# Kernel optimization log

Measured on AMD Instinct MI355X. Metric: run time of the kernel, lower is better.

Reference implementation:

```python
import jax, jax.numpy as jnp
import numpy as np
import math

H, HD = 16, 64
EPS = 1e-6


def setup_inputs() -> dict:
    key = jax.random.key(0)
    ks = jax.random.split(key, 6)
    B, T, D = 4, 2048, 1024
    s = 0.02
    return {
        "x": jax.random.normal(ks[0], (B, T, D), jnp.float32),
        "wq": jax.random.normal(ks[1], (D, D), jnp.float32) * s,
        "wk": jax.random.normal(ks[2], (D, D), jnp.float32) * s,
        "wv": jax.random.normal(ks[3], (D, D), jnp.float32) * s,
        "wo": jax.random.normal(ks[4], (D, D), jnp.float32) * s,
        "norm_g": jnp.ones((D,), jnp.float32),
    }


def reference(x, wq, wk, wv, wo, norm_g):
    B, T, D = x.shape
    scale = math.sqrt(HD)
    # nn.Linear(D, D, bias=False): y = x @ W.T
    q = (x @ wq.T).reshape(B, T, H, HD).transpose(0, 2, 1, 3)  # [B,H,T,HD]
    k = (x @ wk.T).reshape(B, T, H, HD).transpose(0, 2, 1, 3)
    v = (x @ wv.T).reshape(B, T, H, HD).transpose(0, 2, 1, 3)
    scores = jnp.einsum("bhqd,bhkd->bhqk", q, k) / scale  # [B,H,T,T]
    causal = jnp.tril(jnp.ones((T, T), bool))  # True where allowed
    scores = jnp.where(causal, scores, -jnp.inf)
    attn = jax.nn.softmax(scores, axis=-1)  # dropout p=0 -> identity
    out = jnp.einsum("bhqk,bhkd->bhqd", attn, v)  # [B,H,T,HD]
    out = out.transpose(0, 2, 1, 3).reshape(B, T, D)
    y = x + out @ wo.T  # residual
    # RMSNorm
    rms = jnp.sqrt(jnp.mean(y * y, axis=-1, keepdims=True) + EPS)
    return (y / rms) * norm_g
```

## Files before the change

### kernel.cpp

```cpp
#include <hip/hip_runtime.h>
#include <hip/hip_bf16.h>

constexpr int NB  = 4;
constexpr int NT  = 2048;
constexpr int ND  = 1024;
constexpr int NH  = 16;
constexpr int NHD = 64;
constexpr int NM  = NB * NT;

typedef unsigned short u16;
typedef __attribute__((ext_vector_type(8))) short  short8;
typedef __attribute__((ext_vector_type(4))) float  f32x4;

__device__ __forceinline__ u16 f2bf(float f) {
  unsigned u = __builtin_bit_cast(unsigned, f);
  u += 0x7FFFu + ((u >> 16) & 1u);
  return (u16)(u >> 16);
}

__device__ __forceinline__ unsigned pk2bf(float lo, float hi_) {
  float2 t; t.x = lo; t.y = hi_;
  __hip_bfloat162 h2 = __float22bfloat162_rn(t);
  unsigned u;
  __builtin_memcpy(&u, &h2, 4);
  return u;
}

__device__ __forceinline__ void gll16(const u16* src, u16* dst) {
  __builtin_amdgcn_global_load_lds(
      (const __attribute__((address_space(1))) void*)src,
      (__attribute__((address_space(3))) void*)dst, 16, 0, 0);
}

__global__ __launch_bounds__(256) void cast_kernel(const float* __restrict__ in,
                                                   u16* __restrict__ out, int n4) {
  int i = blockIdx.x * 256 + threadIdx.x;
  if (i >= n4) return;
  float4 v = ((const float4*)in)[i];
  ushort4 o;
  o.x = f2bf(v.x); o.y = f2bf(v.y); o.z = f2bf(v.z); o.w = f2bf(v.w);
  ((ushort4*)out)[i] = o;
}

__global__ __launch_bounds__(256) void gemm_qkv(
    const u16* __restrict__ xb,
    const u16* __restrict__ wqb, const u16* __restrict__ wkb, const u16* __restrict__ wvb,
    u16* __restrict__ Qb, u16* __restrict__ Kb, u16* __restrict__ VTb) {
  const int z = blockIdx.z;
  const u16* wsel = (z == 0) ? wqb : (z == 1) ? wkb : wvb;
  u16* osel      = (z == 0) ? Qb  : (z == 1) ? Kb  : VTb;
  const float scl = (z == 0) ? 0.125f * 1.44269504f : 1.0f;

  const int row0 = blockIdx.x * 128;
  const int col0 = blockIdx.y * 128;
  const int tid  = threadIdx.x;
  const int lane = tid & 63, wid = tid >> 6;
  const int wm = wid >> 1, wn = wid & 1;
  const int li = lane & 15, hi = lane >> 4;

  __shared__ __align__(16) u16 lA[128 * 32];
  __shared__ __align__(16) u16 lB[128 * 32];

  f32x4 acc[4][4] = {};
  const int rl = lane >> 2;
  const int c8 = lane & 3;

  for (int k0 = 0; k0 < ND; k0 += 32) {
#pragma unroll
    for (int h = 0; h < 2; ++h) {
      int r = wid * 32 + h * 16 + rl;
      gll16(&xb  [(size_t)(row0 + r) * ND + k0 + c8 * 8], &lA[(wid * 32 + h * 16) * 32]);
      gll16(&wsel[(size_t)(col0 + r) * ND + k0 + c8 * 8], &lB[(wid * 32 + h * 16) * 32]);
    }
    __syncthreads();
    short8 a[4], b[4];
#pragma unroll
    for (int m = 0; m < 4; ++m)
      a[m] = *(const short8*)&lA[(wm * 64 + m * 16 + li) * 32 + hi * 8];
#pragma unroll
    for (int n = 0; n < 4; ++n)
      b[n] = *(const short8*)&lB[(wn * 64 + n * 16 + li) * 32 + hi * 8];
    if (z == 2) {
#pragma unroll
      for (int m = 0; m < 4; ++m)
#pragma unroll
        for (int n = 0; n < 4; ++n)
          acc[m][n] = __builtin_amdgcn_mfma_f32_16x16x32_bf16(a[m], b[n], acc[m][n], 0, 0, 0);
    } else {
#pragma unroll
      for (int m = 0; m < 4; ++m)
#pragma unroll
        for (int n = 0; n < 4; ++n)
          acc[m][n] = __builtin_amdgcn_mfma_f32_16x16x32_bf16(b[n], a[m], acc[m][n], 0, 0, 0);
    }
    __syncthreads();
  }

#pragma unroll
  for (int m = 0; m < 4; ++m)
#pragma unroll
    for (int n = 0; n < 4; ++n) {
      if (z == 2) {
        int token0 = row0 + wm * 64 + m * 16 + hi * 4;
        int col    = col0 + wn * 64 + n * 16 + li;
        int b_ = token0 >> 11, t0 = token0 & (NT - 1);
        int h_ = col >> 6,     d_ = col & (NHD - 1);
        uint2 w;
        w.x = pk2bf(acc[m][n][0], acc[m][n][1]);
        w.y = pk2bf(acc[m][n][2], acc[m][n][3]);
        *(uint2*)&osel[(((size_t)(b_ * NH + h_)) * NHD + d_) * NT + t0] = w;
      } else {
        int token = row0 + wm * 64 + m * 16 + li;
        int feat0 = col0 + wn * 64 + n * 16 + hi * 4;
        int b_ = token >> 11, t_ = token & (NT - 1);
        int h_ = feat0 >> 6,  d0 = feat0 & (NHD - 1);
        uint2 w;
        w.x = pk2bf(acc[m][n][0] * scl, acc[m][n][1] * scl);
        w.y = pk2bf(acc[m][n][2] * scl, acc[m][n][3] * scl);
        *(uint2*)&osel[(((size_t)(b_ * NH + h_)) * NT + t_) * NHD + d0] = w;
      }
    }
}

__global__ __launch_bounds__(256) void gemm_wo(
    const u16* __restrict__ ao, const u16* __restrict__ wob,
    const float* __restrict__ x, float* __restrict__ y) {
  const int row0 = blockIdx.x * 128;
  const int col0 = blockIdx.y * 128;
  const int tid  = threadIdx.x;
  const int lane = tid & 63, wid = tid >> 6;
  const int wm = wid >> 1, wn = wid & 1;
  const int li = lane & 15, hi = lane >> 4;

  __shared__ __align__(16) u16 lA[128 * 32];
  __shared__ __align__(16) u16 lB[128 * 32];

  f32x4 acc[4][4] = {};
  const int rl = lane >> 2;
  const int c8 = lane & 3;

  for (int k0 = 0; k0 < ND; k0 += 32) {
#pragma unroll
    for (int h = 0; h < 2; ++h) {
      int r = wid * 32 + h * 16 + rl;
      gll16(&ao [(size_t)(row0 + r) * ND + k0 + c8 * 8], &lA[(wid * 32 + h * 16) * 32]);
      gll16(&wob[(size_t)(col0 + r) * ND + k0 + c8 * 8], &lB[(wid * 32 + h * 16) * 32]);
    }
    __syncthreads();
    short8 a[4], b[4];
#pragma unroll
    for (int m = 0; m < 4; ++m)
      a[m] = *(const short8*)&lA[(wm * 64 + m * 16 + li) * 32 + hi * 8];
#pragma unroll
    for (int n = 0; n < 4; ++n)
      b[n] = *(const short8*)&lB[(wn * 64 + n * 16 + li) * 32 + hi * 8];
#pragma unroll
    for (int m = 0; m < 4; ++m)
#pragma unroll
      for (int n = 0; n < 4; ++n)
        acc[m][n] = __builtin_amdgcn_mfma_f32_16x16x32_bf16(b[n], a[m], acc[m][n], 0, 0, 0);
    __syncthreads();
  }

#pragma unroll
  for (int m = 0; m < 4; ++m)
#pragma unroll
    for (int n = 0; n < 4; ++n) {
      int token = row0 + wm * 64 + m * 16 + li;
      int feat0 = col0 + wn * 64 + n * 16 + hi * 4;
      size_t idx = (size_t)token * ND + feat0;
      float4 xv = *(const float4*)&x[idx];
      float4 o;
      o.x = acc[m][n][0] + xv.x; o.y = acc[m][n][1] + xv.y;
      o.z = acc[m][n][2] + xv.z; o.w = acc[m][n][3] + xv.w;
      *(float4*)&y[idx] = o;
    }
}

__global__ __launch_bounds__(256) void attn_kernel(
    const u16* __restrict__ Q, const u16* __restrict__ K, const u16* __restrict__ VT,
    u16* __restrict__ AO) {
  const int nb  = gridDim.x * gridDim.y;
  const int b0  = blockIdx.y * gridDim.x + blockIdx.x;
  const int L   = (b0 & 7) * (nb >> 3) + (b0 >> 3);
  const int qb  = 31 - (L & 31);
  const int bh  = L >> 5;

  const int tid = threadIdx.x;
  const int lane = tid & 63, wid = tid >> 6;
  const int li = lane & 15, hi = lane >> 4;
  const int r0 = qb * 64 + wid * 16;
  const int qrow = r0 + li;
  const size_t bK = (size_t)bh * NT * NHD;
  const size_t bV = (size_t)bh * NHD * NT;

  __shared__ __align__(16) u16 lK [2][64 * 64];
  __shared__ __align__(16) u16 lVT[2][64 * 64];
  __shared__ __align__(16) u16 lP [4][16 * 64];

  const int ch0 = tid, ch1 = tid + 256;
  const int d0 = (ch0 >> 3) * 64 + (((ch0 & 7) ^ ((ch0 >> 3) & 7)) << 3);
  const int d1 = (ch1 >> 3) * 64 + (((ch1 & 7) ^ ((ch1 >> 3) & 7)) << 3);
  const int vOff0 = (ch0 >> 3) * NT + (ch0 & 7) * 8;
  const int vOff1 = (ch1 >> 3) * NT + (ch1 & 7) * 8;

  uint4 gK0, gK1, gV0, gV1;
  auto issue = [&](int kt) {
    const u16* kp = K + bK + (size_t)kt * 4096;
    const u16* vp = VT + bV + kt * 64;
    gK0 = *(const uint4*)&kp[ch0 * 8];
    gK1 = *(const uint4*)&kp[ch1 * 8];
    gV0 = *(const uint4*)&vp[vOff0];
    gV1 = *(const uint4*)&vp[vOff1];
  };
  auto commit = [&](int buf) {
    *(uint4*)&lK [buf][d0] = gK0;
    *(uint4*)&lK [buf][d1] = gK1;
    *(uint4*)&lVT[buf][d0] = gV0;
    *(uint4*)&lVT[buf][d1] = gV1;
  };

  short8 qf[2];
#pragma unroll
  for (int c = 0; c < 2; ++c)
    qf[c] = *(const short8*)&Q[bK + (size_t)qrow * NHD + c * 32 + hi * 8];

  short8 vone;
#pragma unroll
  for (int e = 0; e < 8; ++e) vone[e] = (short)0x3F80;

  f32x4 o[4] = {};
  f32x4 o4 = {};
  float mr = -INFINITY;

  issue(0);
  commit(0);
  __syncthreads();
  int buf = 0;

  const int pswz = (li & 7) << 1;

  for (int kt = 0; kt <= qb; ++kt) {
    if (kt < qb) issue(kt + 1);

    f32x4 s[4] = {};
    __builtin_amdgcn_s_setprio(1);
#pragma unroll
    for (int g = 0; g < 4; ++g)
#pragma unroll
      for (int c = 0; c < 2; ++c) {
        short8 kf = *(const short8*)&lK[buf][(g * 16 + li) * 64 + ((c * 4 + hi) ^ (li & 7)) * 8];
        s[g] = __builtin_amdgcn_mfma_f32_16x16x32_bf16(kf, qf[c], s[g], 0, 0, 0);
      }
    __builtin_amdgcn_s_setprio(0);

    if (kt == qb) {
#pragma unroll
      for (int g = 0; g < 4; ++g)
#pragma unroll
        for (int rg = 0; rg < 4; ++rg) {
          int kcol = kt * 64 + g * 16 + hi * 4 + rg;
          if (kcol > qrow) s[g][rg] = -INFINITY;
        }
    }

    float mg0 = fmaxf(fmaxf(s[0][0], s[0][1]), fmaxf(s[0][2], s[0][3]));
    float mg1 = fmaxf(fmaxf(s[1][0], s[1][1]), fmaxf(s[1][2], s[1][3]));
    float mg2 = fmaxf(fmaxf(s[2][0], s[2][1]), fmaxf(s[2][2], s[2][3]));
    float mg3 = fmaxf(fmaxf(s[3][0], s[3][1]), fmaxf(s[3][2], s[3][3]));
    float pmax = fmaxf(fmaxf(mg0, mg1), fmaxf(mg2, mg3));
    pmax = fmaxf(pmax, __shfl_xor(pmax, 16));
    pmax = fmaxf(pmax, __shfl_xor(pmax, 32));

    if (__any(pmax > mr + 8.f)) {
      float mnew = fmaxf(mr, pmax);
      float sc = __builtin_amdgcn_exp2f(mr - mnew);
#pragma unroll
      for (int gd = 0; gd < 4; ++gd)
#pragma unroll
        for (int rg = 0; rg < 4; ++rg) o[gd][rg] *= sc;
#pragma unroll
      for (int rg = 0; rg < 4; ++rg) o4[rg] *= sc;
      mr = mnew;
    }

#pragma unroll
    for (int g = 0; g < 4; ++g) {
      float p0 = __builtin_amdgcn_exp2f(s[g][0] - mr);
      float p1 = __builtin_amdgcn_exp2f(s[g][1] - mr);
      float p2 = __builtin_amdgcn_exp2f(s[g][2] - mr);
      float p3 = __builtin_amdgcn_exp2f(s[g][3] - mr);
      uint2 w;
      w.x = pk2bf(p0, p1);
      w.y = pk2bf(p2, p3);
      int k8s = (g * 4 + hi) ^ pswz;
      *(uint2*)&lP[wid][li * 64 + k8s * 4] = w;
    }

    short8 pa[2];
#pragma unroll
    for (int c = 0; c < 2; ++c)
      pa[c] = *(const short8*)&lP[wid][li * 64 + ((c * 8 + hi * 2) ^ pswz) * 4];

    __builtin_amdgcn_s_setprio(1);
#pragma unroll
    for (int gd = 0; gd < 4; ++gd)
#pragma unroll
      for (int c = 0; c < 2; ++c) {
        short8 vf = *(const short8*)&lVT[buf][(gd * 16 + li) * 64 + ((c * 4 + hi) ^ (li & 7)) * 8];
        o[gd] = __builtin_amdgcn_mfma_f32_16x16x32_bf16(vf, pa[c], o[gd], 0, 0, 0);
      }
#pragma unroll
    for (int c = 0; c < 2; ++c)
      o4 = __builtin_amdgcn_mfma_f32_16x16x32_bf16(vone, pa[c], o4, 0, 0, 0);
    __builtin_amdgcn_s_setprio(0);

    if (kt < qb) commit(buf ^ 1);
    __syncthreads();
    buf ^= 1;
  }

  const int b_ = bh >> 4, h_ = bh & 15;
  const float inv = 1.0f / o4[0];
  const size_t rowbase = ((size_t)(b_ * NT + qrow)) * ND + h_ * 64;
#pragma unroll
  for (int gd = 0; gd < 4; ++gd) {
    uint2 w;
    w.x = pk2bf(o[gd][0] * inv, o[gd][1] * inv);
    w.y = pk2bf(o[gd][2] * inv, o[gd][3] * inv);
    *(uint2*)&AO[rowbase + gd * 16 + hi * 4] = w;
  }
}

__global__ __launch_bounds__(256) void rmsnorm_kernel(float* __restrict__ y,
                                                      const float* __restrict__ g) {
  const int row = blockIdx.x;
  const int tid = threadIdx.x;
  const int lane = tid & 63, wid = tid >> 6;
  float4 v = ((const float4*)(y + (size_t)row * ND))[tid];
  float ss = v.x * v.x + v.y * v.y + v.z * v.z + v.w * v.w;
#pragma unroll
  for (int off = 32; off; off >>= 1) ss += __shfl_down(ss, off);
  __shared__ float red[4];
  if (lane == 0) red[wid] = ss;
  __syncthreads();
  float tot = red[0] + red[1] + red[2] + red[3];
  float inv = rsqrtf(tot * (1.0f / (float)ND) + 1e-6f);
  float4 gg = ((const float4*)g)[tid];
  float4 o;
  o.x = v.x * inv * gg.x; o.y = v.y * inv * gg.y;
  o.z = v.z * inv * gg.z; o.w = v.w * inv * gg.w;
  ((float4*)(y + (size_t)row * ND))[tid] = o;
}

extern "C" void kernel_launch(void* const* d_in, const int* in_sizes, int n_in,
                              void* d_out, int out_size, void* d_ws, size_t ws_size,
                              hipStream_t stream) {
  const float* x  = (const float*)d_in[0];
  const float* wq = (const float*)d_in[1];
  const float* wk = (const float*)d_in[2];
  const float* wv = (const float*)d_in[3];
  const float* wo = (const float*)d_in[4];
  const float* ng = (const float*)d_in[5];
  float* out = (float*)d_out;

  char* ws = (char*)d_ws;
  u16* xb  = (u16*)(ws);
  u16* wqb = (u16*)(ws + (16u << 20));
  u16* wkb = (u16*)(ws + (18u << 20));
  u16* wvb = (u16*)(ws + (20u << 20));
  u16* wob = (u16*)(ws + (22u << 20));
  u16* Qb  = (u16*)(ws + (24u << 20));
  u16* Kb  = (u16*)(ws + (40u << 20));
  u16* VTb = (u16*)(ws + (56u << 20));
  u16* AO  = (u16*)(ws + (72u << 20));

  cast_kernel<<<NM * ND / 4 / 256, 256, 0, stream>>>(x,  xb,  NM * ND / 4);
  cast_kernel<<<ND * ND / 4 / 256, 256, 0, stream>>>(wq, wqb, ND * ND / 4);
  cast_kernel<<<ND * ND / 4 / 256, 256, 0, stream>>>(wk, wkb, ND * ND / 4);
  cast_kernel<<<ND * ND / 4 / 256, 256, 0, stream>>>(wv, wvb, ND * ND / 4);
  cast_kernel<<<ND * ND / 4 / 256, 256, 0, stream>>>(wo, wob, ND * ND / 4);

  gemm_qkv<<<dim3(NM / 128, ND / 128, 3), 256, 0, stream>>>(xb, wqb, wkb, wvb, Qb, Kb, VTb);
  attn_kernel<<<dim3(NT / 64, NB * NH), 256, 0, stream>>>(Qb, Kb, VTb, AO);
  gemm_wo<<<dim3(NM / 128, ND / 128), 256, 0, stream>>>(AO, wob, x, out);
  rmsnorm_kernel<<<NM, 256, 0, stream>>>(out, ng);
}
```

Baseline: 227.0 us.

## Double GEMM K-tile with XOR-swizzled LDS, XCD-aware block remap, fuse weight casts

```diff
diff --git a/kernel.cpp b/kernel.cpp
--- a/kernel.cpp
+++ b/kernel.cpp
@@ -42,56 +42,84 @@
   ((ushort4*)out)[i] = o;
 }
 
+__global__ __launch_bounds__(256) void cast4_kernel(
+    const float* __restrict__ w0, const float* __restrict__ w1,
+    const float* __restrict__ w2, const float* __restrict__ w3,
+    u16* __restrict__ o0, u16* __restrict__ o1,
+    u16* __restrict__ o2, u16* __restrict__ o3) {
+  const int z = blockIdx.x >> 10;
+  const float* in = (z == 0) ? w0 : (z == 1) ? w1 : (z == 2) ? w2 : w3;
+  u16* out       = (z == 0) ? o0 : (z == 1) ? o1 : (z == 2) ? o2 : o3;
+  int i = (blockIdx.x & 1023) * 256 + threadIdx.x;
+  float4 v = ((const float4*)in)[i];
+  ushort4 o;
+  o.x = f2bf(v.x); o.y = f2bf(v.y); o.z = f2bf(v.z); o.w = f2bf(v.w);
+  ((ushort4*)out)[i] = o;
+}
+
 __global__ __launch_bounds__(256) void gemm_qkv(
     const u16* __restrict__ xb,
     const u16* __restrict__ wqb, const u16* __restrict__ wkb, const u16* __restrict__ wvb,
     u16* __restrict__ Qb, u16* __restrict__ Kb, u16* __restrict__ VTb) {
-  const int z = blockIdx.z;
+  const int nwg  = 64 * 8 * 3;
+  const int flat = (blockIdx.z * 8 + blockIdx.y) * 64 + blockIdx.x;
+  const int L    = (flat & 7) * (nwg >> 3) + (flat >> 3);
+  const int z    = L / 512;
+  const int rem  = L & 511;
+  const int col0 = (rem >> 6) << 7;
+  const int row0 = (rem & 63) << 7;
+
   const u16* wsel = (z == 0) ? wqb : (z == 1) ? wkb : wvb;
   u16* osel      = (z == 0) ? Qb  : (z == 1) ? Kb  : VTb;
   const float scl = (z == 0) ? 0.125f * 1.44269504f : 1.0f;
 
-  const int row0 = blockIdx.x * 128;
-  const int col0 = blockIdx.y * 128;
   const int tid  = threadIdx.x;
   const int lane = tid & 63, wid = tid >> 6;
   const int wm = wid >> 1, wn = wid & 1;
   const int li = lane & 15, hi = lane >> 4;
-
-  __shared__ __align__(16) u16 lA[128 * 32];
-  __shared__ __align__(16) u16 lB[128 * 32];
+  const int rl8 = lane >> 3, sl = lane & 7;
+
+  __shared__ __align__(16) u16 lA[128 * 64];
+  __shared__ __align__(16) u16 lB[128 * 64];
 
   f32x4 acc[4][4] = {};
-  const int rl = lane >> 2;
-  const int c8 = lane & 3;
-
-  for (int k0 = 0; k0 < ND; k0 += 32) {
-#pragma unroll
-    for (int h = 0; h < 2; ++h) {
-      int r = wid * 32 + h * 16 + rl;
-      gll16(&xb  [(size_t)(row0 + r) * ND + k0 + c8 * 8], &lA[(wid * 32 + h * 16) * 32]);
-      gll16(&wsel[(size_t)(col0 + r) * ND + k0 + c8 * 8], &lB[(wid * 32 + h * 16) * 32]);
+
+  for (int k0 = 0; k0 < ND; k0 += 64) {
+#pragma unroll
+    for (int h = 0; h < 4; ++h) {
+      int r  = wid * 32 + h * 8 + rl8;
+      int cs = ((sl ^ (r & 7)) << 3);
+      gll16(&xb  [(size_t)(row0 + r) * ND + k0 + cs], &lA[(wid * 32 + h * 8) * 64]);
+      gll16(&wsel[(size_t)(col0 + r) * ND + k0 + cs], &lB[(wid * 32 + h * 8) * 64]);
     }
     __syncthreads();
-    short8 a[4], b[4];
+    short8 a[4][2], b[4][2];
 #pragma unroll
     for (int m = 0; m < 4; ++m)
-      a[m] = *(const short8*)&lA[(wm * 64 + m * 16 + li) * 32 + hi * 8];
+#pragma unroll
+      for (int c = 0; c < 2; ++c)
+        a[m][c] = *(const short8*)&lA[(wm * 64 + m * 16 + li) * 64 + (((c * 4 + hi) ^ (li & 7)) << 3)];
 #pragma unroll
     for (int n = 0; n < 4; ++n)
-      b[n] = *(const short8*)&lB[(wn * 64 + n * 16 + li) * 32 + hi * 8];
+#pragma unroll
+      for (int c = 0; c < 2; ++c)
+        b[n][c] = *(const short8*)&lB[(wn * 64 + n * 16 + li) * 64 + (((c * 4 + hi) ^ (li & 7)) << 3)];
     if (z == 2) {
 #pragma unroll
       for (int m = 0; m < 4; ++m)
 #pragma unroll
         for (int n = 0; n < 4; ++n)
-          acc[m][n] = __builtin_amdgcn_mfma_f32_16x16x32_bf16(a[m], b[n], acc[m][n], 0, 0, 0);
+#pragma unroll
+          for (int c = 0; c < 2; ++c)
+            acc[m][n] = __builtin_amdgcn_mfma_f32_16x16x32_bf16(a[m][c], b[n][c], acc[m][n], 0, 0, 0);
     } else {
 #pragma unroll
       for (int m = 0; m < 4; ++m)
 #pragma unroll
         for (int n = 0; n < 4; ++n)
-          acc[m][n] = __builtin_amdgcn_mfma_f32_16x16x32_bf16(b[n], a[m], acc[m][n], 0, 0, 0);
+#pragma unroll
+          for (int c = 0; c < 2; ++c)
+            acc[m][n] = __builtin_amdgcn_mfma_f32_16x16x32_bf16(b[n][c], a[m][c], acc[m][n], 0, 0, 0);
     }
     __syncthreads();
   }
@@ -125,40 +153,50 @@
 __global__ __launch_bounds__(256) void gemm_wo(
     const u16* __restrict__ ao, const u16* __restrict__ wob,
     const float* __restrict__ x, float* __restrict__ y) {
-  const int row0 = blockIdx.x * 128;
-  const int col0 = blockIdx.y * 128;
+  const int nwg  = 64 * 8;
+  const int flat = blockIdx.y * 64 + blockIdx.x;
+  const int L    = (flat & 7) * (nwg >> 3) + (flat >> 3);
+  const int col0 = (L >> 6) << 7;
+  const int row0 = (L & 63) << 7;
+
   const int tid  = threadIdx.x;
   const int lane = tid & 63, wid = tid >> 6;
   const int wm = wid >> 1, wn = wid & 1;
   const int li = lane & 15, hi = lane >> 4;
-
-  __shared__ __align__(16) u16 lA[128 * 32];
-  __shared__ __align__(16) u16 lB[128 * 32];
+  const int rl8 = lane >> 3, sl = lane & 7;
+
+  __shared__ __align__(16) u16 lA[128 * 64];
+  __shared__ __align__(16) u16 lB[128 * 64];
 
   f32x4 acc[4][4] = {};
-  const int rl = lane >> 2;
-  const int c8 = lane & 3;
-
-  for (int k0 = 0; k0 < ND; k0 += 32) {
-#pragma unroll
-    for (int h = 0; h < 2; ++h) {
-      int r = wid * 32 + h * 16 + rl;
-      gll16(&ao [(size_t)(row0 + r) * ND + k0 + c8 * 8], &lA[(wid * 32 + h * 16) * 32]);
-      gll16(&wob[(size_t)(col0 + r) * ND + k0 + c8 * 8], &lB[(wid * 32 + h * 16) * 32]);
+
+  for (int k0 = 0; k0 < ND; k0 += 64) {
+#pragma unroll
+    for (int h = 0; h < 4; ++h) {
+      int r  = wid * 32 + h * 8 + rl8;
+      int cs = ((sl ^ (r & 7)) << 3);
+      gll16(&ao [(size_t)(row0 + r) * ND + k0 + cs], &lA[(wid * 32 + h * 8) * 64]);
+      gll16(&wob[(size_t)(col0 + r) * ND + k0 + cs], &lB[(wid * 32 + h * 8) * 64]);
     }
     __syncthreads();
-    short8 a[4], b[4];
+    short8 a[4][2], b[4][2];
 #pragma unroll
     for (int m = 0; m < 4; ++m)
-      a[m] = *(const short8*)&lA[(wm * 64 + m * 16 + li) * 32 + hi * 8];
+#pragma unroll
+      for (int c = 0; c < 2; ++c)
+        a[m][c] = *(const short8*)&lA[(wm * 64 + m * 16 + li) * 64 + (((c * 4 + hi) ^ (li & 7)) << 3)];
 #pragma unroll
     for (int n = 0; n < 4; ++n)
-      b[n] = *(const short8*)&lB[(wn * 64 + n * 16 + li) * 32 + hi * 8];
+#pragma unroll
+      for (int c = 0; c < 2; ++c)
+        b[n][c] = *(const short8*)&lB[(wn * 64 + n * 16 + li) * 64 + (((c * 4 + hi) ^ (li & 7)) << 3)];
 #pragma unroll
     for (int m = 0; m < 4; ++m)
 #pragma unroll
       for (int n = 0; n < 4; ++n)
-        acc[m][n] = __builtin_amdgcn_mfma_f32_16x16x32_bf16(b[n], a[m], acc[m][n], 0, 0, 0);
+#pragma unroll
+        for (int c = 0; c < 2; ++c)
+          acc[m][n] = __builtin_amdgcn_mfma_f32_16x16x32_bf16(b[n][c], a[m][c], acc[m][n], 0, 0, 0);
     __syncthreads();
   }
 
@@ -375,14 +413,11 @@
   u16* VTb = (u16*)(ws + (56u << 20));
   u16* AO  = (u16*)(ws + (72u << 20));
 
-  cast_kernel<<<NM * ND / 4 / 256, 256, 0, stream>>>(x,  xb,  NM * ND / 4);
-  cast_kernel<<<ND * ND / 4 / 256, 256, 0, stream>>>(wq, wqb, ND * ND / 4);
-  cast_kernel<<<ND * ND / 4 / 256, 256, 0, stream>>>(wk, wkb, ND * ND / 4);
-  cast_kernel<<<ND * ND / 4 / 256, 256, 0, stream>>>(wv, wvb, ND * ND / 4);
-  cast_kernel<<<ND * ND / 4 / 256, 256, 0, stream>>>(wo, wob, ND * ND / 4);
-
-  gemm_qkv<<<dim3(NM / 128, ND / 128, 3), 256, 0, stream>>>(xb, wqb, wkb, wvb, Qb, Kb, VTb);
+  cast_kernel<<<NM * ND / 4 / 256, 256, 0, stream>>>(x, xb, NM * ND / 4);
+  cast4_kernel<<<4 * 1024, 256, 0, stream>>>(wq, wk, wv, wo, wqb, wkb, wvb, wob);
+
+  gemm_qkv<<<dim3(64, 8, 3), 256, 0, stream>>>(xb, wqb, wkb, wvb, Qb, Kb, VTb);
   attn_kernel<<<dim3(NT / 64, NB * NH), 256, 0, stream>>>(Qb, Kb, VTb, AO);
-  gemm_wo<<<dim3(NM / 128, ND / 128), 256, 0, stream>>>(AO, wob, x, out);
+  gemm_wo<<<dim3(64, 8), 256, 0, stream>>>(AO, wob, x, out);
   rmsnorm_kernel<<<NM, 256, 0, stream>>>(out, ng);
 }
```

Measured after the change: 219.3 us. -3.4%, faster.
